# Optimization experiments

Hardware: AMD Instinct MI355X
Metric: run time of the kernel (lower is better)

The kernel has to match this reference:

```python
import jax, jax.numpy as jnp
import numpy as np

N, C, H, W = 4, 256, 64, 64
S = 2          # scale_factor
K = 5          # up_kernel
G = 1          # up_group
CK = 64        # compressed_channels


def conv2d(x, w, b, pad):
    out = jax.lax.conv_general_dilated(
        x, w, window_strides=(1, 1), padding=[(pad, pad), (pad, pad)],
        dimension_numbers=('NCHW', 'OIHW', 'NCHW'))
    return out + b[None, :, None, None]


def pixel_shuffle(x, r):
    n, cr, h, w = x.shape
    c = cr // (r * r)
    return x.reshape(n, c, r, r, h, w).transpose(0, 1, 4, 2, 5, 3).reshape(n, c, h * r, w * r)


def grid_sample_border(img, grid):
    # img [N,C,Hi,Wi], grid [N,Ho,Wo,2] in [-1,1] (x,y); bilinear, border pad, align_corners=True
    n, c, hi, wi = img.shape
    gx = (grid[..., 0] + 1.0) * 0.5 * (wi - 1)
    gy = (grid[..., 1] + 1.0) * 0.5 * (hi - 1)
    gx = jnp.clip(gx, 0.0, wi - 1.0)
    gy = jnp.clip(gy, 0.0, hi - 1.0)
    x0 = jnp.floor(gx).astype(jnp.int32)
    y0 = jnp.floor(gy).astype(jnp.int32)
    x1 = jnp.minimum(x0 + 1, wi - 1)
    y1 = jnp.minimum(y0 + 1, hi - 1)
    wx = (gx - x0)[..., None]
    wy = (gy - y0)[..., None]
    bidx = jnp.arange(n)[:, None, None]
    def gather(yy, xx):
        return img[bidx, :, yy, xx]  # [N,Ho,Wo,C]
    v00 = gather(y0, x0)
    v01 = gather(y0, x1)
    v10 = gather(y1, x0)
    v11 = gather(y1, x1)
    out = (v00 * (1 - wx) * (1 - wy) + v01 * wx * (1 - wy)
           + v10 * (1 - wx) * wy + v11 * wx * wy)
    return out.transpose(0, 3, 1, 2)


def carafe2(features, masks, k, g, up):
    n, c, h, w = features.shape
    cg = c // g
    k2 = k * k
    # masks [N, g*k2, h*up, w*up] -> per-pixel kernels [n,g,h,w,k2,up2]
    m = masks.reshape(n, g, k2, h, up, w, up)
    m = m.transpose(0, 1, 2, 3, 5, 4, 6).reshape(n, g, k2, h, w, up * up)
    kern = m.transpose(0, 1, 3, 4, 2, 5)            # [n,g,h,w,k2,up2]
    f = features.reshape(n, g, cg, h, w)
    p = k // 2
    fp = jnp.pad(f, ((0, 0), (0, 0), (0, 0), (p, p), (p, p)))
    patches = jnp.stack([fp[:, :, :, i:i + h, j:j + w]
                         for i in range(k) for j in range(k)], axis=-1)  # [n,g,cg,h,w,k2]
    xp = patches.transpose(0, 1, 3, 4, 2, 5)        # [n,g,h,w,cg,k2]
    out = jnp.einsum('nghwck,nghwku->nghwcu', xp, kern)  # [n,g,h,w,cg,up2]
    out = out.transpose(0, 1, 4, 2, 3, 5).reshape(n, c * up * up, h, w)
    return pixel_shuffle(out, up)


def setup_inputs() -> dict:
    key = jax.random.key(0)
    ks = jax.random.split(key, 4)
    x = jax.random.normal(ks[0], (N, C, H, W), dtype=jnp.float32)
    w_comp = jax.random.normal(ks[1], (CK, C, 1, 1), dtype=jnp.float32) * 0.05
    b_comp = jnp.zeros((CK,), dtype=jnp.float32)
    w_ker = jax.random.normal(ks[2], (G * K * K, CK, 3, 3), dtype=jnp.float32) * 0.001
    b_ker = jnp.zeros((G * K * K,), dtype=jnp.float32)
    w_off = jax.random.normal(ks[3], (G * 2 * S * S, CK, 3, 3), dtype=jnp.float32) * 0.01
    b_off = jnp.zeros((G * 2 * S * S,), dtype=jnp.float32)
    return {'x': x, 'w_comp': w_comp, 'b_comp': b_comp,
            'w_ker': w_ker, 'b_ker': b_ker, 'w_off': w_off, 'b_off': b_off}


def reference(x, w_comp, b_comp, w_ker, b_ker, w_off, b_off):
    cx = conv2d(x, w_comp, b_comp, 0)               # channel compressor (1x1)
    offset = conv2d(cx, w_off, b_off, 1)            # [N, 2*S*S, H, W]
    mask = conv2d(cx, w_ker, b_ker, 1)              # [N, G*K*K, H, W]
    # kernel_space_normalizer: softmax over the K*K kernel positions
    n, mc, h, w = mask.shape
    mask = jax.nn.softmax(mask.reshape(n, mc // (K * K), K * K, h, w), axis=2)
    mask = mask.reshape(n, mc, h, w)
    # kernel_space_expander
    off = pixel_shuffle(offset, S).transpose(0, 2, 3, 1)  # [N, H*S, W*S, 2]
    off = off * jnp.array([2.0 / (w - 1), 2.0 / (h - 1)], dtype=off.dtype)
    gh = jnp.repeat(jnp.linspace(-1.0, 1.0, h), S)  # [H*S]
    gw = jnp.repeat(jnp.linspace(-1.0, 1.0, w), S)  # [W*S]
    base = jnp.stack(jnp.broadcast_arrays(gw[None, :], gh[:, None]), axis=-1)  # [H*S, W*S, 2]
    grid = base[None] + off
    mask_ = grid_sample_border(mask, grid)          # [N, G*K*K, H*S, W*S]
    return carafe2(x, mask_, K, G, S)
```

## Files before the change

kernel.cpp:

```cpp
#include <hip/hip_runtime.h>
#include <math.h>

#define NB 4
#define C_IN 256
#define CKC 64
#define HWSZ 4096
#define K2 25
#define NOC2 40

#define WS_CX    0
#define WS_OFF   (WS_CX + NB*CKC*HWSZ)
#define WS_MASK  (WS_OFF + NB*8*HWSZ)
#define WS_WT    (WS_MASK + NB*K2*HWSZ)

#define NWT (CKC * 9 * NOC2)
#define NWC (C_IN * CKC)

__global__ void k_wt(const float* __restrict__ wk, const float* __restrict__ wo,
                     const float* __restrict__ wc,
                     float* __restrict__ wT, float* __restrict__ wcT) {
  int i = blockIdx.x * 256 + threadIdx.x;
  if (i < NWT) {
    int oc = i % NOC2;
    int r = i / NOC2;
    int tap = r % 9, c = r / 9;
    float v = 0.f;
    if (oc < 8)       v = wo[(oc * CKC + c) * 9 + tap];
    else if (oc < 33) v = wk[((oc - 8) * CKC + c) * 9 + tap];
    wT[i] = v;
  } else {
    int j = i - NWT;
    if (j < NWC) {
      int c = j >> 6, ck = j & 63;
      wcT[j] = wc[ck * C_IN + c];
    }
  }
}

__global__ __launch_bounds__(512) void k_cs(const float* __restrict__ x,
    const float* __restrict__ wcT, const float* __restrict__ bc,
    const float* __restrict__ wT, const float* __restrict__ bk, const float* __restrict__ bo,
    float* __restrict__ offb, float* __restrict__ maskb) {
  __attribute__((aligned(16))) __shared__ float s_mem[9216];
  float* s_tile = s_mem;
  float* s_res  = s_mem;

  int t = threadIdx.x;
  int n = blockIdx.y;
  int tile = blockIdx.x;
  int x0 = (tile & 3) * 16, y0 = (tile >> 2) * 4;
  const float* xn = x + (size_t)n * (C_IN * HWSZ);

  int srcOff[4];
  unsigned vbits = 0, wbits = 0;
  #pragma unroll
  for (int it = 0; it < 4; it++) {
    int e = t + it * 512;
    int c = e / 60;
    int rem = e - c * 60;
    int row = rem / 10, pr = rem - row * 10;
    int gy = y0 - 1 + row;
    int gc0 = x0 - 2 + pr * 2;
    bool wr = (e < 1920);
    bool ok = wr & ((unsigned)gy < 64u) & ((unsigned)gc0 < 63u);
    srcOff[it] = ok ? (c * HWSZ + gy * 64 + gc0) : 0;
    vbits |= (ok ? 1u : 0u) << it;
    wbits |= (wr ? 1u : 0u) << it;
  }

  float2 rv[4];
  #pragma unroll
  for (int it = 0; it < 4; it++) rv[it] = *(const float2*)(xn + srcOff[it]);

  int p = t & 63;
  int g = __builtin_amdgcn_readfirstlane(t >> 6);
  int q1 = p + 60;
  int q1c = (q1 < 120) ? q1 : 119;
  int r0q = p / 20,  c0q = p - r0q * 20;
  int r1q = q1c / 20, c1q = q1c - r1q * 20;
  bool val0 = (c0q >= 1) & (c0q <= 18);
  bool val1 = (q1 < 120) & (c1q >= 1) & (c1q <= 18);
  int toff0 = r0q * 24 + c0q - 1;
  int toff1 = r1q * 24 + c1q - 1;
  float a0[8], a1[8];
  #pragma unroll
  for (int i = 0; i < 8; i++) { a0[i] = bc[g * 8 + i]; a1[i] = a0[i]; }

  float* sA = s_mem;
  float* sB = s_mem + 3840;
  #pragma unroll
  for (int it = 0; it < 4; it++)
    if (wbits & (1u << it))
      *(float2*)(&sA[2 * t + it * 1024]) =
          (vbits & (1u << it)) ? rv[it] : make_float2(0.f, 0.f);
  {
    const float* xb = xn + (size_t)32 * HWSZ;
    #pragma unroll
    for (int it = 0; it < 4; it++) rv[it] = *(const float2*)(xb + srcOff[it]);
  }
  __syncthreads();

  for (int hc = 0; hc < 8; hc++) {
    if (hc < 7) {
      #pragma unroll
      for (int it = 0; it < 4; it++)
        if (wbits & (1u << it))
          *(float2*)(&sB[2 * t + it * 1024]) =
              (vbits & (1u << it)) ? rv[it] : make_float2(0.f, 0.f);
    }
    if (hc < 6) {
      const float* xb = xn + (size_t)(hc + 2) * 32 * HWSZ;
      #pragma unroll
      for (int it = 0; it < 4; it++) rv[it] = *(const float2*)(xb + srcOff[it]);
    }
    const float* wbase = wcT + (hc * 32) * 64 + g * 8;
    #pragma unroll 4
    for (int c = 0; c < 32; c++) {
      float v0 = sA[c * 120 + p];
      float v1 = sA[c * 120 + q1c];
      const float* w = wbase + c * 64;
      #pragma unroll
      for (int i = 0; i < 8; i++) { a0[i] += v0 * w[i]; a1[i] += v1 * w[i]; }
    }
    __syncthreads();
    float* tmp = sA; sA = sB; sB = tmp;
  }

  if (val0) {
    #pragma unroll
    for (int i = 0; i < 8; i++) s_tile[(g * 8 + i) * 144 + toff0] = a0[i];
  }
  if (val1) {
    #pragma unroll
    for (int i = 0; i < 8; i++) s_tile[(g * 8 + i) * 144 + toff1] = a1[i];
  }
  __syncthreads();

  int px = p & 15, py = p >> 4;
  float acc[5];
  #pragma unroll
  for (int j = 0; j < 5; j++) acc[j] = 0.f;
  const float* wg = wT + g * 5;
  const float* tl0 = s_tile + py * 24 + px;

#define LOADWIN(dst, cidx)                                   \
  {                                                          \
    const float* tlc = tl0 + (cidx) * 144;                   \
    _Pragma("unroll")                                        \
    for (int tap = 0; tap < 9; tap++) {                      \
      int dy = tap / 3, dx = tap % 3;                        \
      dst[tap] = tlc[dy * 24 + dx];                          \
    }                                                        \
  }
#define FMAWIN(src, cidx)                                    \
  {                                                          \
    const float* wc9 = wg + (cidx) * 9 * NOC2;               \
    _Pragma("unroll")                                        \
    for (int tap = 0; tap < 9; tap++) {                      \
      float v = src[tap];                                    \
      const float* w = wc9 + tap * NOC2;                     \
      _Pragma("unroll")                                      \
      for (int j = 0; j < 5; j++) acc[j] += v * w[j];        \
    }                                                        \
  }

  float wa[9], wbuf[9];
  LOADWIN(wa, 0)
  LOADWIN(wbuf, 1)
  #pragma unroll 1
  for (int c = 0; c < CKC; c += 2) {
    FMAWIN(wa, c)
    if (c + 2 < CKC) LOADWIN(wa, c + 2)
    FMAWIN(wbuf, c + 1)
    if (c + 3 < CKC) LOADWIN(wbuf, c + 3)
  }
#undef LOADWIN
#undef FMAWIN

  __syncthreads();
  #pragma unroll
  for (int j = 0; j < 5; j++) s_res[(g * 5 + j) * 64 + p] = acc[j];
  __syncthreads();

  int hw = (y0 + py) * 64 + x0 + px;
  offb[(n * 8 + g) * HWSZ + hw] = s_res[g * 64 + p] + bo[g];
  if (t < 64) {
    float m[25], mx = -1e30f;
    #pragma unroll
    for (int k = 0; k < 25; k++) { m[k] = s_res[(8 + k) * 64 + p] + bk[k]; mx = fmaxf(mx, m[k]); }
    float s = 0.f;
    #pragma unroll
    for (int k = 0; k < 25; k++) { m[k] = __expf(m[k] - mx); s += m[k]; }
    float inv = 1.f / s;
    #pragma unroll
    for (int k = 0; k < 25; k++) maskb[(n * 25 + k) * HWSZ + hw] = m[k] * inv;
  }
}

__global__ __launch_bounds__(256, 4) void k_carafe(const float* __restrict__ x,
    const float* __restrict__ offb, const float* __restrict__ maskb,
    float* __restrict__ out) {
  __attribute__((aligned(16))) __shared__ float s_patch[32 * 202];
  __attribute__((aligned(16))) __shared__ float s_kern[32 * 25 * 4];
  int t = threadIdx.x;
  int b = blockIdx.x;
  int n = b >> 8;
  int r = b & 255;
  int half = r & 1;
  int wq = (r >> 1) & 3;
  int aa = r >> 3;
  int a = aa + (aa & 16);
  int yout = (a & 15) * 8 + wq * 2 + ((a >> 5) & 1);
  int w0 = wq * 16;
  int cbase = n * C_IN + half * 128;

  int srcOff[13];
  int dstOff[13];
  unsigned vbits = 0;
  unsigned wbits = 0;
  #pragma unroll
  for (int it = 0; it < 13; it++) {
    int e = t + it * 256;
    int c = e / 100;
    int rem = e - c * 100;
    int rg = rem / 10;
    int c2 = rem - rg * 10;
    int row = (rg < 5) ? (a - 2 + rg) : (a + 9 + rg);
    int gc0 = w0 - 2 + c2 * 2;
    bool wr = (e < 3200);
    bool ok = wr & ((unsigned)row < 64u) & ((unsigned)gc0 < 64u);
    srcOff[it] = ok ? (c * HWSZ + row * 64 + gc0) : 0;
    dstOff[it] = wr ? 2 * (e + c) : 0;
    vbits |= (ok ? 1u : 0u) << it;
    wbits |= (wr ? 1u : 0u) << it;
  }

  float2 rv[13];
  {
    const float* xn = x + (size_t)cbase * HWSZ;
    #pragma unroll
    for (int it = 0; it < 13; it++) rv[it] = *(const float2*)(xn + srcOff[it]);
  }

  if (t < 128) {
    int p = t >> 2, u = t & 3;
    int hb = p >> 4, wl = p & 15;
    int h = a + hb * 16;
    int wcol = w0 + wl;
    float ox = offb[(n * 8 + u) * HWSZ + h * 64 + wcol];
    float oy = offb[(n * 8 + 4 + u) * HWSZ + h * 64 + wcol];
    float gx = fminf(fmaxf((float)wcol + ox, 0.f), 63.f);
    float gy = fminf(fmaxf((float)h + oy, 0.f), 63.f);
    float fx0 = floorf(gx), fy0 = floorf(gy);
    int x0 = (int)fx0, y0 = (int)fy0;
    float fx = gx - fx0, fy = gy - fy0;
    int x1 = min(x0 + 1, 63), y1 = min(y0 + 1, 63);
    float w11 = fx * fy;
    float w10 = fy - w11, w01 = fx - w11, w00 = 1.f - fx - fy + w11;
    const float* mb = maskb + n * (K2 * HWSZ);
    int i00 = y0 * 64 + x0, i01 = y0 * 64 + x1;
    int i10 = y1 * 64 + x0, i11 = y1 * 64 + x1;
    #pragma unroll 5
    for (int k = 0; k < 25; k++) {
      const float* mk = mb + k * HWSZ;
      float v = w00 * mk[i00] + w01 * mk[i01] + w10 * mk[i10] + w11 * mk[i11];
      s_kern[(p * 25 + k) * 4 + u] = v;
    }
  }

  int cl = t & 31, g = t >> 5;
  int hb = g >> 2, wl0 = (g & 3) * 4;
  float* s_out = s_patch;

  for (int cc = 0; cc < 4; cc++) {
    __syncthreads();
    #pragma unroll
    for (int it = 0; it < 13; it++) {
      if (wbits & (1u << it)) {
        float2 v = (vbits & (1u << it)) ? rv[it] : make_float2(0.f, 0.f);
        *(float2*)(&s_patch[dstOff[it]]) = v;
      }
    }
    __syncthreads();
    if (cc < 3) {
      const float* xn = x + (size_t)(cbase + (cc + 1) * 32) * HWSZ;
      #pragma unroll
      for (int it = 0; it < 13; it++) rv[it] = *(const float2*)(xn + srcOff[it]);
    }
    float acc[4][4];
    #pragma unroll
    for (int i = 0; i < 4; i++)
      acc[i][0] = acc[i][1] = acc[i][2] = acc[i][3] = 0.f;
    const float* pc = s_patch + cl * 202 + hb * 100 + wl0;
    #pragma unroll
    for (int dy = 0; dy < 5; dy++) {
      float r8[8];
      #pragma unroll
      for (int j = 0; j < 8; j++) r8[j] = pc[dy * 20 + j];
      #pragma unroll
      for (int pr = 0; pr < 4; pr++) {
        const float4* kp = (const float4*)(s_kern + (((g * 4 + pr) * 25) + dy * 5) * 4);
        #pragma unroll
        for (int dx = 0; dx < 5; dx++) {
          float f = r8[pr + dx];
          float4 k4 = kp[dx];
          acc[pr][0] += f * k4.x;
          acc[pr][1] += f * k4.y;
          acc[pr][2] += f * k4.z;
          acc[pr][3] += f * k4.w;
        }
      }
    }
    __syncthreads();
    #pragma unroll
    for (int pr = 0; pr < 4; pr++) {
      int wl = wl0 + pr;
      #pragma unroll
      for (int u = 0; u < 4; u++) {
        int xo = wl * 8 + u * 2 + hb;
        s_out[cl * 130 + xo] = acc[pr][u];
      }
    }
    __syncthreads();
    float* obase = out + ((size_t)(cbase + cc * 32) * 128 + yout) * 128;
    #pragma unroll
    for (int it = 0; it < 4; it++) {
      int q2 = t + it * 256;
      int rowc = q2 >> 5;
      int col4 = q2 & 31;
      const float* sp = s_out + rowc * 130 + col4 * 4;
      float4 v = make_float4(sp[0], sp[1], sp[2], sp[3]);
      *(float4*)(obase + (size_t)rowc * (128 * 128) + col4 * 4) = v;
    }
  }
}

extern "C" void kernel_launch(void* const* d_in, const int* in_sizes, int n_in,
                              void* d_out, int out_size, void* d_ws, size_t ws_size,
                              hipStream_t stream) {
  const float* x      = (const float*)d_in[0];
  const float* w_comp = (const float*)d_in[1];
  const float* b_comp = (const float*)d_in[2];
  const float* w_ker  = (const float*)d_in[3];
  const float* b_ker  = (const float*)d_in[4];
  const float* w_off  = (const float*)d_in[5];
  const float* b_off  = (const float*)d_in[6];
  float* out = (float*)d_out;
  float* ws = (float*)d_ws;
  float* offb  = ws + WS_OFF;
  float* maskb = ws + WS_MASK;
  float* wT    = ws + WS_WT;
  float* wcT   = ws + WS_CX;

  hipLaunchKernelGGL(k_wt, dim3((NWT + NWC + 255) / 256), dim3(256), 0, stream,
                     w_ker, w_off, w_comp, wT, wcT);
  hipLaunchKernelGGL(k_cs, dim3(64, 4), dim3(512), 0, stream,
                     x, wcT, b_comp, wT, b_ker, b_off, offb, maskb);
  hipLaunchKernelGGL(k_carafe, dim3(1024), dim3(256), 0, stream, x, offb, maskb, out);
}
```

Measured before the change: 183.1 us.

## Split k_cs channel reductions across two wave groups in 1024-thread blocks

Doubles the k_cs block to 1024 threads and splits the channel reductions between two wave halves. The 1x1 compressor now stages 64 input channels per round, and each half accumulates only its assigned rounds. The 3x3 offset/mask conv is split over 32 compressed channels per half. Partial sums are combined through LDS with extra barriers, aiming to raise occupancy and latency hiding on the 256-block grid. The trade-off is more shared memory, extra synchronisation, and compressor rounds where half the waves sit idle.

Measured after the change: 173.0 us, median of 2. 1.06x faster.

```diff
diff --git a/kernel.cpp b/kernel.cpp
--- a/kernel.cpp
+++ b/kernel.cpp
@@ -37,11 +37,11 @@
   }
 }
 
-__global__ __launch_bounds__(512) void k_cs(const float* __restrict__ x,
+__global__ __launch_bounds__(1024) void k_cs(const float* __restrict__ x,
     const float* __restrict__ wcT, const float* __restrict__ bc,
     const float* __restrict__ wT, const float* __restrict__ bk, const float* __restrict__ bo,
     float* __restrict__ offb, float* __restrict__ maskb) {
-  __attribute__((aligned(16))) __shared__ float s_mem[9216];
+  __attribute__((aligned(16))) __shared__ float s_mem[15360];
   float* s_tile = s_mem;
   float* s_res  = s_mem;
 
@@ -51,29 +51,28 @@
   int x0 = (tile & 3) * 16, y0 = (tile >> 2) * 4;
   const float* xn = x + (size_t)n * (C_IN * HWSZ);
 
+  int p = t & 63;
+  int w = t >> 6;
+  int g = __builtin_amdgcn_readfirstlane(w & 7);
+  int ch = __builtin_amdgcn_readfirstlane(w >> 3);
+
   int srcOff[4];
   unsigned vbits = 0, wbits = 0;
   #pragma unroll
   for (int it = 0; it < 4; it++) {
-    int e = t + it * 512;
+    int e = t + it * 1024;
     int c = e / 60;
     int rem = e - c * 60;
     int row = rem / 10, pr = rem - row * 10;
     int gy = y0 - 1 + row;
     int gc0 = x0 - 2 + pr * 2;
-    bool wr = (e < 1920);
+    bool wr = (e < 3840);
     bool ok = wr & ((unsigned)gy < 64u) & ((unsigned)gc0 < 63u);
     srcOff[it] = ok ? (c * HWSZ + gy * 64 + gc0) : 0;
     vbits |= (ok ? 1u : 0u) << it;
     wbits |= (wr ? 1u : 0u) << it;
   }
 
-  float2 rv[4];
-  #pragma unroll
-  for (int it = 0; it < 4; it++) rv[it] = *(const float2*)(xn + srcOff[it]);
-
-  int p = t & 63;
-  int g = __builtin_amdgcn_readfirstlane(t >> 6);
   int q1 = p + 60;
   int q1c = (q1 < 120) ? q1 : 119;
   int r0q = p / 20,  c0q = p - r0q * 20;
@@ -84,55 +83,83 @@
   int toff1 = r1q * 24 + c1q - 1;
   float a0[8], a1[8];
   #pragma unroll
-  for (int i = 0; i < 8; i++) { a0[i] = bc[g * 8 + i]; a1[i] = a0[i]; }
+  for (int i = 0; i < 8; i++) {
+    float b = (ch == 0) ? bc[g * 8 + i] : 0.f;
+    a0[i] = b; a1[i] = b;
+  }
+
+  float2 rv[4];
+  #pragma unroll
+  for (int it = 0; it < 4; it++) rv[it] = *(const float2*)(xn + srcOff[it]);
 
   float* sA = s_mem;
-  float* sB = s_mem + 3840;
+  float* sB = s_mem + 7680;
   #pragma unroll
   for (int it = 0; it < 4; it++)
     if (wbits & (1u << it))
-      *(float2*)(&sA[2 * t + it * 1024]) =
+      *(float2*)(&sA[2 * t + it * 2048]) =
           (vbits & (1u << it)) ? rv[it] : make_float2(0.f, 0.f);
   {
-    const float* xb = xn + (size_t)32 * HWSZ;
+    const float* xb = xn + (size_t)64 * HWSZ;
     #pragma unroll
     for (int it = 0; it < 4; it++) rv[it] = *(const float2*)(xb + srcOff[it]);
   }
   __syncthreads();
 
-  for (int hc = 0; hc < 8; hc++) {
-    if (hc < 7) {
+  for (int k = 0; k < 4; k++) {
+    if (k < 3) {
       #pragma unroll
       for (int it = 0; it < 4; it++)
         if (wbits & (1u << it))
-          *(float2*)(&sB[2 * t + it * 1024]) =
+          *(float2*)(&sB[2 * t + it * 2048]) =
               (vbits & (1u << it)) ? rv[it] : make_float2(0.f, 0.f);
     }
-    if (hc < 6) {
-      const float* xb = xn + (size_t)(hc + 2) * 32 * HWSZ;
+    if (k < 2) {
+      const float* xb = xn + (size_t)(k + 2) * 64 * HWSZ;
       #pragma unroll
       for (int it = 0; it < 4; it++) rv[it] = *(const float2*)(xb + srcOff[it]);
     }
-    const float* wbase = wcT + (hc * 32) * 64 + g * 8;
-    #pragma unroll 4
-    for (int c = 0; c < 32; c++) {
-      float v0 = sA[c * 120 + p];
-      float v1 = sA[c * 120 + q1c];
-      const float* w = wbase + c * 64;
-      #pragma unroll
-      for (int i = 0; i < 8; i++) { a0[i] += v0 * w[i]; a1[i] += v1 * w[i]; }
+    if ((k >> 1) == ch) {
+      const float* wbase = wcT + (k * 64) * 64 + g * 8;
+      #pragma unroll 4
+      for (int c = 0; c < 64; c++) {
+        float v0 = sA[c * 120 + p];
+        float v1 = sA[c * 120 + q1c];
+        const float* wp = wbase + c * 64;
+        #pragma unroll
+        for (int i = 0; i < 8; i++) { a0[i] += v0 * wp[i]; a1[i] += v1 * wp[i]; }
+      }
     }
     __syncthreads();
     float* tmp = sA; sA = sB; sB = tmp;
   }
 
-  if (val0) {
-    #pragma unroll
-    for (int i = 0; i < 8; i++) s_tile[(g * 8 + i) * 144 + toff0] = a0[i];
-  }
-  if (val1) {
-    #pragma unroll
-    for (int i = 0; i < 8; i++) s_tile[(g * 8 + i) * 144 + toff1] = a1[i];
+  if (ch == 1) {
+    if (val0) {
+      #pragma unroll
+      for (int i = 0; i < 8; i++) s_tile[(g * 8 + i) * 144 + toff0] = a0[i];
+    }
+    if (val1) {
+      #pragma unroll
+      for (int i = 0; i < 8; i++) s_tile[(g * 8 + i) * 144 + toff1] = a1[i];
+    }
+  }
+  __syncthreads();
+  if (ch == 0) {
+    if (val0) {
+      #pragma unroll
+      for (int i = 0; i < 8; i++) {
+        int idx = (g * 8 + i) * 144 + toff0;
+        s_tile[idx] = s_tile[idx] + a0[i];
+      }
+    }
+    if (val1) {
+      #pragma unroll
+      for (int i = 0; i < 8; i++) {
+        int idx = (g * 8 + i) * 144 + toff1;
+        s_tile[idx] = s_tile[idx] + a1[i];
+      }
+    }
   }
   __syncthreads();
 
@@ -142,6 +169,7 @@
   for (int j = 0; j < 5; j++) acc[j] = 0.f;
   const float* wg = wT + g * 5;
   const float* tl0 = s_tile + py * 24 + px;
+  int cb = ch * 32;
 
 #define LOADWIN(dst, cidx)                                   \
   {                                                          \
@@ -158,32 +186,40 @@
     _Pragma("unroll")                                        \
     for (int tap = 0; tap < 9; tap++) {                      \
       float v = src[tap];                                    \
-      const float* w = wc9 + tap * NOC2;                     \
+      const float* wp = wc9 + tap * NOC2;                    \
       _Pragma("unroll")                                      \
-      for (int j = 0; j < 5; j++) acc[j] += v * w[j];        \
+      for (int j = 0; j < 5; j++) acc[j] += v * wp[j];       \
     }                                                        \
   }
 
   float wa[9], wbuf[9];
-  LOADWIN(wa, 0)
-  LOADWIN(wbuf, 1)
+  LOADWIN(wa, cb + 0)
+  LOADWIN(wbuf, cb + 1)
   #pragma unroll 1
-  for (int c = 0; c < CKC; c += 2) {
-    FMAWIN(wa, c)
-    if (c + 2 < CKC) LOADWIN(wa, c + 2)
-    FMAWIN(wbuf, c + 1)
-    if (c + 3 < CKC) LOADWIN(wbuf, c + 3)
+  for (int c = 0; c < 32; c += 2) {
+    FMAWIN(wa, cb + c)
+    if (c + 2 < 32) LOADWIN(wa, cb + c + 2)
+    FMAWIN(wbuf, cb + c + 1)
+    if (c + 3 < 32) LOADWIN(wbuf, cb + c + 3)
   }
 #undef LOADWIN
 #undef FMAWIN
 
   __syncthreads();
-  #pragma unroll
-  for (int j = 0; j < 5; j++) s_res[(g * 5 + j) * 64 + p] = acc[j];
+  if (ch == 0) {
+    #pragma unroll
+    for (int j = 0; j < 5; j++) s_res[(g * 5 + j) * 64 + p] = acc[j];
+  }
+  __syncthreads();
+  if (ch == 1) {
+    #pragma unroll
+    for (int j = 0; j < 5; j++) s_res[(g * 5 + j) * 64 + p] += acc[j];
+  }
   __syncthreads();
 
   int hw = (y0 + py) * 64 + x0 + px;
-  offb[(n * 8 + g) * HWSZ + hw] = s_res[g * 64 + p] + bo[g];
+  if (ch == 0)
+    offb[(n * 8 + g) * HWSZ + hw] = s_res[g * 64 + p] + bo[g];
   if (t < 64) {
     float m[25], mx = -1e30f;
     #pragma unroll
@@ -354,7 +390,7 @@
 
   hipLaunchKernelGGL(k_wt, dim3((NWT + NWC + 255) / 256), dim3(256), 0, stream,
                      w_ker, w_off, w_comp, wT, wcT);
-  hipLaunchKernelGGL(k_cs, dim3(64, 4), dim3(512), 0, stream,
+  hipLaunchKernelGGL(k_cs, dim3(64, 4), dim3(1024), 0, stream,
                      x, wcT, b_comp, wT, b_ker, b_off, offb, maskb);
   hipLaunchKernelGGL(k_carafe, dim3(1024), dim3(256), 0, stream, x, offb, maskb, out);
 }
```
